# Kernel tuning notes

Hardware: AMD Instinct MI355X
Metric: run time of the kernel (lower is better)

Reference implementation:

```python
import jax, jax.numpy as jnp
import numpy as np

B, S, H, DH, HQ, HKV = 2, 1024, 2048, 128, 16, 4
E, K, I, IS = 16, 4, 1024, 1024
EPS = 1e-5
ROPE_BASE = 10000.0
ROUTED_SCALE = 1.0


def rmsnorm(x, w):
    v = jnp.mean(x.astype(jnp.float32) ** 2, axis=-1, keepdims=True)
    return (x.astype(jnp.float32) * jax.lax.rsqrt(v + EPS)).astype(x.dtype) * w


def rope(x, cos, sin):
    x1, x2 = jnp.split(x, 2, axis=-1)
    return jnp.concatenate([x1 * cos - x2 * sin, x2 * cos + x1 * sin], axis=-1)


def setup_inputs() -> dict:
    key = jax.random.key(0)
    ks = jax.random.split(key, 24)
    s = 0.02
    inp = {}
    inp['x'] = jax.random.normal(ks[0], (B, S, H), dtype=jnp.float32)
    inp['in_ln_w'] = jnp.ones((H,), jnp.float32)
    inp['wq'] = jax.random.normal(ks[1], (H, HQ * DH), jnp.float32) * s
    inp['bq'] = jax.random.normal(ks[2], (HQ * DH,), jnp.float32) * s
    inp['wk'] = jax.random.normal(ks[3], (H, HKV * DH), jnp.float32) * s
    inp['bk'] = jax.random.normal(ks[4], (HKV * DH,), jnp.float32) * s
    inp['wv'] = jax.random.normal(ks[5], (H, HKV * DH), jnp.float32) * s
    inp['bv'] = jax.random.normal(ks[6], (HKV * DH,), jnp.float32) * s
    inp['qn_w'] = jnp.ones((DH,), jnp.float32)
    inp['kn_w'] = jnp.ones((DH,), jnp.float32)
    inp['wo'] = jax.random.normal(ks[7], (HQ * DH, H), jnp.float32) * s
    inp['post_ln_w'] = jnp.ones((H,), jnp.float32)
    inp['gate_w'] = jax.random.normal(ks[8], (E, H), jnp.float32) * s
    inp['gate_b'] = jax.random.normal(ks[9], (E,), jnp.float32) * s
    inp['wg'] = jax.random.normal(ks[10], (E, H, I), jnp.float32) * s
    inp['wu'] = jax.random.normal(ks[11], (E, H, I), jnp.float32) * s
    inp['wd'] = jax.random.normal(ks[12], (E, I, H), jnp.float32) * s
    inp['swg'] = jax.random.normal(ks[13], (H, IS), jnp.float32) * s
    inp['swu'] = jax.random.normal(ks[14], (H, IS), jnp.float32) * s
    inp['swd'] = jax.random.normal(ks[15], (IS, H), jnp.float32) * s
    return inp


def reference(x, in_ln_w, wq, bq, wk, bk, wv, bv, qn_w, kn_w, wo, post_ln_w,
              gate_w, gate_b, wg, wu, wd, swg, swu, swd):
    # ---- attention block ----
    res = x
    h = rmsnorm(x, in_ln_w)
    q = (h @ wq + bq).reshape(B, S, HQ, DH)
    k = (h @ wk + bk).reshape(B, S, HKV, DH)
    v = (h @ wv + bv).reshape(B, S, HKV, DH)
    q = rmsnorm(q, qn_w)  # per-head QK norm over head_dim
    k = rmsnorm(k, kn_w)
    inv_freq = 1.0 / (ROPE_BASE ** (jnp.arange(0, DH, 2, dtype=jnp.float32) / DH))  # [DH/2]
    fr = jnp.arange(S, dtype=jnp.float32)[:, None] * inv_freq[None, :]  # [S, DH/2]
    cos = jnp.cos(fr)[None, :, None, :]
    sin = jnp.sin(fr)[None, :, None, :]
    q = rope(q, cos, sin)
    k = rope(k, cos, sin)
    g = HQ // HKV
    k = jnp.repeat(k, g, axis=2)  # GQA expand to [B,S,HQ,DH]
    v = jnp.repeat(v, g, axis=2)
    scores = jnp.einsum('bqhd,bkhd->bhqk', q, k) * (DH ** -0.5)
    causal = jnp.tril(jnp.ones((S, S), dtype=bool))
    scores = jnp.where(causal[None, None], scores, jnp.float32(-1e30))
    attn = jax.nn.softmax(scores, axis=-1)
    o = jnp.einsum('bhqk,bkhd->bqhd', attn, v).reshape(B, S, HQ * DH) @ wo
    x = res + o
    # ---- MoE block ----
    res = x
    h = rmsnorm(x, post_ln_w)
    ht = h.reshape(B * S, H)  # [T, H]
    logits = ht.astype(jnp.float32) @ gate_w.T  # fp32 router
    scr = jax.nn.sigmoid(logits)  # [T, E]
    choice = scr + gate_b[None, :]  # noaux_tc: bias only for selection
    _, topi = jax.lax.top_k(choice, K)  # [T, K]
    tw = jnp.take_along_axis(scr, topi, axis=-1)  # unbiased combine weights
    tw = tw / (jnp.sum(tw, axis=-1, keepdims=True) + 1e-20)  # norm_topk_prob
    tw = tw * ROUTED_SCALE
    cw = jnp.sum(jax.nn.one_hot(topi, E, dtype=jnp.float32) * tw[..., None], axis=1)  # [T, E]
    a = jnp.einsum('th,ehi->eti', ht, wg)
    b = jnp.einsum('th,ehi->eti', ht, wu)
    inter = jax.nn.silu(a) * b * cw.T[:, :, None]  # scale before down-proj
    routed = jnp.einsum('eti,eih->th', inter, wd)
    shared = (jax.nn.silu(ht @ swg) * (ht @ swu)) @ swd
    out = res + (routed + shared).reshape(B, S, H)
    return out
```

## Files before the change

### kernel.cpp

```cpp
#include <hip/hip_runtime.h>
#include <math.h>

typedef unsigned short u16;
typedef __attribute__((ext_vector_type(8))) short short8;
typedef __attribute__((ext_vector_type(4))) float f32x4;

#define B_ 2
#define S_ 1024
#define H_ 2048
#define DH_ 128
#define HQ_ 16
#define HKV_ 4
#define E_ 16
#define TOPK_ 4
#define I_ 1024
#define T_ (B_*S_)
#define NQKV_ 3072
#define NSEG_ 17
#define NA_ (T_*TOPK_ + T_)
#define K3_ 6144
#define MAXTILE 97

#define QPLANE ((long)B_*HQ_*S_*DH_)
#define KPLANE ((long)B_*HKV_*S_*DH_)
#define VPLANE ((long)B_*HKV_*DH_*S_)

__device__ __forceinline__ float bf2f(u16 u){
  union { unsigned int i; float f; } x; x.i = ((unsigned int)u) << 16; return x.f;
}
__device__ __forceinline__ u16 f2bf(float f){
  union { float f; unsigned int i; } x; x.f = f;
  unsigned int r = x.i + 0x7fffu + ((x.i >> 16) & 1u);
  return (u16)(r >> 16);
}
__device__ __forceinline__ void split_bf(float v, u16& hi, u16& lo){
  hi = f2bf(v);
  lo = f2bf(v - bf2f(hi));
}

__device__ __forceinline__ void gld_lds16(const void* g, void* l){
  __builtin_amdgcn_global_load_lds(
      (const __attribute__((address_space(1))) unsigned int*)g,
      (__attribute__((address_space(3))) unsigned int*)l, 16, 0, 0);
}

__device__ __forceinline__ f32x4 mfma_bf16(short8 a, short8 b, f32x4 c){
  return __builtin_amdgcn_mfma_f32_16x16x32_bf16(a, b, c, 0, 0, 0);
}

__global__ void k_transpose(const float* __restrict__ in, u16* __restrict__ out,
                            int R, int C, int rowMul, int rowOff,
                            long inBatch, long outBatch, int split3)
{
  __shared__ float tile[64][65];
  const float* inp = in + (long)blockIdx.z * inBatch;
  u16* outp = out + (long)blockIdx.z * outBatch;
  int c0 = blockIdx.x * 64, r0 = blockIdx.y * 64;
  int tid = threadIdx.x;
  int qc = (tid & 15) * 4;
  int rr = tid >> 4;
#pragma unroll
  for (int p = 0; p < 4; p++){
    int r = p*16 + rr;
    float4 v = *(const float4*)(inp + (long)(r0 + r)*C + c0 + qc);
    tile[r][qc] = v.x; tile[r][qc+1] = v.y; tile[r][qc+2] = v.z; tile[r][qc+3] = v.w;
  }
  __syncthreads();
  int rl = (tid & 15) * 4;
  int cw = tid >> 4;
#pragma unroll
  for (int p = 0; p < 4; p++){
    int c = p*16 + cw;
    float v0 = tile[rl][c], v1 = tile[rl+1][c], v2 = tile[rl+2][c], v3 = tile[rl+3][c];
    if (split3){
      ushort4 hi, lo;
      split_bf(v0, hi.x, lo.x); split_bf(v1, hi.y, lo.y);
      split_bf(v2, hi.z, lo.z); split_bf(v3, hi.w, lo.w);
      long base = (long)((c0 + c)*rowMul + rowOff) * (3*R) + r0 + rl;
      *(ushort4*)(outp + base)       = hi;
      *(ushort4*)(outp + base + R)   = lo;
      *(ushort4*)(outp + base + 2*R) = hi;
    } else {
      ushort4 hi = { f2bf(v0), f2bf(v1), f2bf(v2), f2bf(v3) };
      *(ushort4*)(outp + (long)((c0 + c)*rowMul + rowOff) * R + r0 + rl) = hi;
    }
  }
}

__global__ void k_rmsnorm(const float* __restrict__ x, const float* __restrict__ w,
                          u16* __restrict__ out3)
{
  int t = blockIdx.x;
  const float4* r4 = (const float4*)(x + (long)t * H_);
  const float4* w4 = (const float4*)w;
  float4 a = r4[threadIdx.x], b = r4[threadIdx.x + 256];
  float ss = a.x*a.x + a.y*a.y + a.z*a.z + a.w*a.w
           + b.x*b.x + b.y*b.y + b.z*b.z + b.w*b.w;
#pragma unroll
  for (int d = 1; d < 64; d <<= 1) ss += __shfl_xor(ss, d);
  __shared__ float red[4];
  int lane = threadIdx.x & 63, wv = threadIdx.x >> 6;
  if (lane == 0) red[wv] = ss;
  __syncthreads();
  ss = red[0] + red[1] + red[2] + red[3];
  float rs = rsqrtf(ss * (1.f / 2048.f) + 1e-5f);
  float4 wa = w4[threadIdx.x], wb = w4[threadIdx.x + 256];
  float va[8] = { a.x*rs*wa.x, a.y*rs*wa.y, a.z*rs*wa.z, a.w*rs*wa.w,
                  b.x*rs*wb.x, b.y*rs*wb.y, b.z*rs*wb.z, b.w*rs*wb.w };
  int pos0 = threadIdx.x*4, pos1 = 1024 + threadIdx.x*4;
  ushort4 hi0, lo0, hi1, lo1;
  split_bf(va[0], hi0.x, lo0.x); split_bf(va[1], hi0.y, lo0.y);
  split_bf(va[2], hi0.z, lo0.z); split_bf(va[3], hi0.w, lo0.w);
  split_bf(va[4], hi1.x, lo1.x); split_bf(va[5], hi1.y, lo1.y);
  split_bf(va[6], hi1.z, lo1.z); split_bf(va[7], hi1.w, lo1.w);
  u16* row = out3 + (long)t * K3_;
  *(ushort4*)(row + pos0) = hi0;        *(ushort4*)(row + pos1) = hi1;
  *(ushort4*)(row + 2048 + pos0) = hi0; *(ushort4*)(row + 2048 + pos1) = hi1;
  *(ushort4*)(row + 4096 + pos0) = lo0; *(ushort4*)(row + 4096 + pos1) = lo1;
}

__global__ void k_add_rmsnorm(const float* __restrict__ x, const float* __restrict__ p0,
                              const float* __restrict__ w, float* __restrict__ xa,
                              u16* __restrict__ out1, float* __restrict__ outf)
{
  int t = blockIdx.x;
  long base = (long)t * H_;
  const float4* x4 = (const float4*)(x + base);
  const float4* a4 = (const float4*)(p0 + base);
  const float4* w4 = (const float4*)w;
  int i0 = threadIdx.x, i1 = threadIdx.x + 256;
  float4 xv0 = x4[i0], xv1 = x4[i1];
  float4 av0 = a4[i0], av1 = a4[i1];
  float4 s0, s1;
  s0.x = xv0.x+av0.x; s0.y = xv0.y+av0.y; s0.z = xv0.z+av0.z; s0.w = xv0.w+av0.w;
  s1.x = xv1.x+av1.x; s1.y = xv1.y+av1.y; s1.z = xv1.z+av1.z; s1.w = xv1.w+av1.w;
  *(float4*)(xa + base + i0*4) = s0;
  *(float4*)(xa + base + i1*4) = s1;
  float ss = s0.x*s0.x + s0.y*s0.y + s0.z*s0.z + s0.w*s0.w
           + s1.x*s1.x + s1.y*s1.y + s1.z*s1.z + s1.w*s1.w;
#pragma unroll
  for (int d = 1; d < 64; d <<= 1) ss += __shfl_xor(ss, d);
  __shared__ float red[4];
  int lane = threadIdx.x & 63, wv = threadIdx.x >> 6;
  if (lane == 0) red[wv] = ss;
  __syncthreads();
  ss = red[0] + red[1] + red[2] + red[3];
  float rs = rsqrtf(ss * (1.f / 2048.f) + 1e-5f);
  float4 wa = w4[i0], wb = w4[i1];
  float va[8] = { s0.x*rs*wa.x, s0.y*rs*wa.y, s0.z*rs*wa.z, s0.w*rs*wa.w,
                  s1.x*rs*wb.x, s1.y*rs*wb.y, s1.z*rs*wb.z, s1.w*rs*wb.w };
  ushort4 q0 = { f2bf(va[0]), f2bf(va[1]), f2bf(va[2]), f2bf(va[3]) };
  ushort4 q1 = { f2bf(va[4]), f2bf(va[5]), f2bf(va[6]), f2bf(va[7]) };
  *(ushort4*)(out1 + base + i0*4) = q0;
  *(ushort4*)(out1 + base + i1*4) = q1;
  float4 oa = { va[0], va[1], va[2], va[3] };
  float4 ob = { va[4], va[5], va[6], va[7] };
  *(float4*)(outf + base + i0*4) = oa;
  *(float4*)(outf + base + i1*4) = ob;
}

__global__ void k_ropetab(float* __restrict__ tab){
  int s = blockIdx.x, i = threadIdx.x;
  double inv = pow(10000.0, -(double)i / 64.0);
  double fr = (double)s * inv;
  tab[s*128 + i]      = (float)cos(fr);
  tab[s*128 + 64 + i] = (float)sin(fr);
}

__global__ void k_ropenorm(const float* __restrict__ qkv, const float* __restrict__ biascat,
                           const float* __restrict__ qnw, const float* __restrict__ knw,
                           const float* __restrict__ tab,
                           u16* __restrict__ Q, u16* __restrict__ Kn, u16* __restrict__ Vt)
{
  long gw = (long)blockIdx.x * 4 + (threadIdx.x >> 6);
  int lane = threadIdx.x & 63;
  int hr = (int)(gw % 24);
  long bs = gw / 24;
  int s = (int)(bs % S_);
  int b = (int)(bs / S_);
  long ro = bs * NQKV_ + hr * DH_;
  float x1 = qkv[ro + lane] + biascat[hr*DH_ + lane];
  float x2 = qkv[ro + lane + 64] + biascat[hr*DH_ + lane + 64];
  if (hr < 20){
    float ss = x1*x1 + x2*x2;
#pragma unroll
    for (int d = 1; d < 64; d <<= 1) ss += __shfl_xor(ss, d);
    float rs = rsqrtf(ss * (1.f/128.f) + 1e-5f);
    const float* wn = (hr < 16) ? qnw : knw;
    float y1 = x1 * rs * wn[lane], y2 = x2 * rs * wn[lane + 64];
    float c = tab[s*128 + lane], sn = tab[s*128 + 64 + lane];
    float o1 = y1*c - y2*sn, o2 = y2*c + y1*sn;
    if (hr < 16){
      const float sc = 0.088388347648318447f;
      u16 h1,l1,h2,l2;
      split_bf(o1*sc, h1, l1); split_bf(o2*sc, h2, l2);
      u16* dst = Q + (((long)b*HQ_ + hr)*S_ + s) * DH_;
      dst[lane] = h1; dst[lane+64] = h2;
      dst[QPLANE + lane] = l1; dst[QPLANE + lane+64] = l2;
    } else {
      u16 h1,l1,h2,l2;
      split_bf(o1, h1, l1); split_bf(o2, h2, l2);
      u16* dst = Kn + (((long)b*HKV_ + (hr-16))*S_ + s) * DH_;
      dst[lane] = h1; dst[lane+64] = h2;
      dst[KPLANE + lane] = l1; dst[KPLANE + lane+64] = l2;
    }
  } else {
    u16 h1,l1,h2,l2;
    split_bf(x1, h1, l1); split_bf(x2, h2, l2);
    u16* dst = Vt + (((long)b*HKV_ + (hr-20))*DH_) * S_ + s;
    dst[(long)lane * S_]        = h1;
    dst[(long)(lane + 64) * S_] = h2;
    dst[VPLANE + (long)lane * S_]        = l1;
    dst[VPLANE + (long)(lane + 64) * S_] = l2;
  }
}

__launch_bounds__(256)
__global__ void k_attn(const u16* __restrict__ Q, const u16* __restrict__ Kn,
                       const u16* __restrict__ Vt, u16* __restrict__ O3)
{
  __shared__ u16 Ksh[32][128];
  __shared__ u16 Ksl[32][128];
  __shared__ u16 Vsh[128][32];
  __shared__ u16 Vsl[128][32];
  __shared__ u16 Psh[4][16][40];
  __shared__ u16 Psl[4][16][40];
  int qb = blockIdx.x, h = blockIdx.y, b = blockIdx.z;
  int kvh = h >> 2;
  int q0 = qb * 64;
  int tid = threadIdx.x, lane = tid & 63, w = tid >> 6;

  const u16* Qg = Q  + (((long)b*HQ_  + h  )*S_ + q0) * DH_;
  const u16* Kg = Kn + (((long)b*HKV_ + kvh)*S_) * DH_;
  const u16* Vg = Vt + (((long)b*HKV_ + kvh)*DH_) * S_;

  short8 qh[4], ql[4];
  {
    long qrow = w*16 + (lane & 15);
    int coff = (lane >> 4) << 3;
#pragma unroll
    for (int kst = 0; kst < 4; kst++){
      qh[kst] = *(const short8*)(Qg + qrow*DH_ + kst*32 + coff);
      ql[kst] = *(const short8*)(Qg + QPLANE + qrow*DH_ + kst*32 + coff);
    }
  }

  f32x4 o[8];
#pragma unroll
  for (int nt = 0; nt < 8; nt++) o[nt] = (f32x4){0.f,0.f,0.f,0.f};
  float mrow[4] = {-INFINITY,-INFINITY,-INFINITY,-INFINITY};
  float lrow[4] = {0.f,0.f,0.f,0.f};

  for (int j = 0; j <= 2*qb + 1; ++j){
#pragma unroll
    for (int it = 0; it < 2; ++it){
      int flat = it*256 + tid;
      int r = flat >> 4, pc = flat & 15;
      int c = pc ^ (((r&7) << 1) | ((r >> 3) & 1));
      long gsrc = ((long)(j*32 + r))*DH_ + c*8;
      gld_lds16(Kg + gsrc,          &Ksh[0][0] + (it*256 + (w<<6))*8);
      gld_lds16(Kg + KPLANE + gsrc, &Ksl[0][0] + (it*256 + (w<<6))*8);
    }
#pragma unroll
    for (int it = 0; it < 2; ++it){
      int flat = it*256 + tid;
      int r = flat >> 2, pc = flat & 3;
      int c = pc ^ (r & 3);
      long gsrc = (long)r*S_ + j*32 + c*8;
      gld_lds16(Vg + gsrc,          &Vsh[0][0] + (it*256 + (w<<6))*8);
      gld_lds16(Vg + VPLANE + gsrc, &Vsl[0][0] + (it*256 + (w<<6))*8);
    }
    __syncthreads();

    f32x4 s[2];
#pragma unroll
    for (int nt = 0; nt < 2; nt++) s[nt] = (f32x4){0.f,0.f,0.f,0.f};
#pragma unroll
    for (int kst = 0; kst < 4; kst++){
#pragma unroll
      for (int nt = 0; nt < 2; nt++){
        int br = nt*16 + (lane & 15);
        int bc = (kst*4 + (lane >> 4)) ^ (((br&7)<<1) | ((br>>3)&1));
        short8 kh = *(const short8*)&Ksh[br][bc*8];
        short8 kl = *(const short8*)&Ksl[br][bc*8];
        s[nt] = mfma_bf16(qh[kst], kh, s[nt]);
        s[nt] = mfma_bf16(qh[kst], kl, s[nt]);
        s[nt] = mfma_bf16(ql[kst], kh, s[nt]);
      }
    }
    if (j >= 2*qb){
#pragma unroll
      for (int nt = 0; nt < 2; nt++){
        int key = j*32 + nt*16 + (lane & 15);
#pragma unroll
        for (int r = 0; r < 4; r++){
          int qrow = q0 + w*16 + ((lane >> 4) << 2) + r;
          if (key > qrow) s[nt][r] = -1e30f;
        }
      }
    }
    float pm[4];
#pragma unroll
    for (int r = 0; r < 4; r++) pm[r] = fmaxf(s[0][r], s[1][r]);
#pragma unroll
    for (int d = 1; d < 16; d <<= 1){
#pragma unroll
      for (int r = 0; r < 4; r++) pm[r] = fmaxf(pm[r], __shfl_xor(pm[r], d));
    }
    float alpha[4];
#pragma unroll
    for (int r = 0; r < 4; r++){
      float mn = fmaxf(mrow[r], pm[r]);
      alpha[r] = __expf(mrow[r] - mn);
      mrow[r] = mn;
    }
    float psum[4] = {0.f,0.f,0.f,0.f};
#pragma unroll
    for (int nt = 0; nt < 2; nt++){
#pragma unroll
      for (int r = 0; r < 4; r++){
        float p = __expf(s[nt][r] - mrow[r]);
        psum[r] += p;
        u16 ph, pl; split_bf(p, ph, pl);
        int qr = ((lane>>4)<<2) + r, kc = nt*16 + (lane & 15);
        Psh[w][qr][kc] = ph;
        Psl[w][qr][kc] = pl;
      }
    }
#pragma unroll
    for (int d = 1; d < 16; d <<= 1){
#pragma unroll
      for (int r = 0; r < 4; r++) psum[r] += __shfl_xor(psum[r], d);
    }
#pragma unroll
    for (int r = 0; r < 4; r++) lrow[r] = lrow[r]*alpha[r] + psum[r];
#pragma unroll
    for (int nt = 0; nt < 8; nt++)
#pragma unroll
      for (int r = 0; r < 4; r++) o[nt][r] *= alpha[r];

    {
      short8 pah = *(const short8*)&Psh[w][lane & 15][(lane >> 4) << 3];
      short8 pal = *(const short8*)&Psl[w][lane & 15][(lane >> 4) << 3];
#pragma unroll
      for (int nt = 0; nt < 8; nt++){
        int br = nt*16 + (lane & 15);
        int bc = (lane >> 4) ^ (br & 3);
        short8 vh = *(const short8*)&Vsh[br][bc*8];
        short8 vl = *(const short8*)&Vsl[br][bc*8];
        o[nt] = mfma_bf16(pah, vh, o[nt]);
        o[nt] = mfma_bf16(pah, vl, o[nt]);
        o[nt] = mfma_bf16(pal, vh, o[nt]);
      }
    }
    __syncthreads();
  }
  float inv_[4];
#pragma unroll
  for (int r = 0; r < 4; r++) inv_[r] = 1.f / lrow[r];
#pragma unroll
  for (int nt = 0; nt < 8; nt++){
#pragma unroll
    for (int r = 0; r < 4; r++){
      long row = (long)b*S_ + q0 + w*16 + ((lane >> 4) << 2) + r;
      float val = o[nt][r] * inv_[r];
      u16 hi, lo; split_bf(val, hi, lo);
      long base = row*K3_ + h*DH_ + nt*16 + (lane & 15);
      O3[base]        = hi;
      O3[base + 2048] = hi;
      O3[base + 4096] = lo;
    }
  }
}

template<int KITERS>
__launch_bounds__(256)
__global__ void k_gemm_d(const u16* __restrict__ A, const u16* __restrict__ Bm,
                         float* __restrict__ C, int N, int Kstride)
{
  __shared__ u16 LDS[4*8192];
  int tid = threadIdx.x;
  int lane = tid & 63, w = tid >> 6;
  int wr = w >> 1, wc = w & 1;
  int n0 = blockIdx.x * 128;
  int m0 = blockIdx.y * 128;

  const u16* aS[2]; const u16* bS[2];
#pragma unroll
  for (int it = 0; it < 2; ++it){
    int c = w + it*4;
    int row = c*16 + (lane >> 2);
    int ps = (lane & 3) ^ ((row >> 1) & 3);
    aS[it] = A + (long)(m0 + row) * Kstride + ps*8;
    bS[it] = Bm + (long)(n0 + row) * Kstride + ps*8;
  }

  int offA[4], offB[4];
#pragma unroll
  for (int m = 0; m < 4; m++){
    int r = wr*64 + m*16 + (lane & 15);
    int ps = (lane >> 4) ^ ((r >> 1) & 3);
    offA[m] = r*32 + ps*8;
  }
#pragma unroll
  for (int n = 0; n < 4; n++){
    int r = wc*64 + n*16 + (lane & 15);
    int ps = (lane >> 4) ^ ((r >> 1) & 3);
    offB[n] = 4096 + r*32 + ps*8;
  }

  f32x4 acc[4][4];
#pragma unroll
  for (int m = 0; m < 4; m++)
#pragma unroll
    for (int n = 0; n < 4; n++) acc[m][n] = (f32x4){0.f,0.f,0.f,0.f};

  auto STAGE = [&](int Tt){
    int kb = Tt * 32;
    int db = (Tt & 3) * 8192;
#pragma unroll
    for (int it = 0; it < 2; ++it){
      gld_lds16(aS[it] + kb, &LDS[db + (w + it*4)*512]);
      gld_lds16(bS[it] + kb, &LDS[db + 4096 + (w + it*4)*512]);
    }
  };

  STAGE(0); STAGE(1); STAGE(2);

  for (int T = 0; T < KITERS; ++T){
    if (T + 3 < KITERS) STAGE(T + 3);
    int rem = KITERS - 1 - T;
    if (rem >= 3)      asm volatile("s_waitcnt vmcnt(12)" ::: "memory");
    else if (rem == 2) asm volatile("s_waitcnt vmcnt(8)"  ::: "memory");
    else if (rem == 1) asm volatile("s_waitcnt vmcnt(4)"  ::: "memory");
    else               asm volatile("s_waitcnt vmcnt(0)"  ::: "memory");
    __builtin_amdgcn_s_barrier();
    __builtin_amdgcn_sched_barrier(0);
    const u16* L = &LDS[(T & 3) * 8192];
    short8 af[4], bfv[4];
#pragma unroll
    for (int m = 0; m < 4; m++) af[m]  = *(const short8*)(L + offA[m]);
#pragma unroll
    for (int n = 0; n < 4; n++) bfv[n] = *(const short8*)(L + offB[n]);
#pragma unroll
    for (int m = 0; m < 4; m++)
#pragma unroll
      for (int n = 0; n < 4; n++)
        acc[m][n] = mfma_bf16(af[m], bfv[n], acc[m][n]);
    asm volatile("s_waitcnt lgkmcnt(0)" ::: "memory");
    __builtin_amdgcn_sched_barrier(0);
    __builtin_amdgcn_s_barrier();
  }

#pragma unroll
  for (int m = 0; m < 4; m++){
    int row0 = m0 + wr*64 + m*16 + ((lane >> 4) << 2);
#pragma unroll
    for (int n = 0; n < 4; n++){
      int col = n0 + wc*64 + n*16 + (lane & 15);
#pragma unroll
      for (int r = 0; r < 4; r++)
        C[(long)(row0 + r)*N + col] = acc[m][n][r];
    }
  }
}

template<int MODE>
__launch_bounds__(256)
__global__ void k_gemm_g(const u16* __restrict__ A, const u16* __restrict__ Bm,
                         void* __restrict__ Cout,
                         int Kloop, long segStrideB,
                         const int* __restrict__ segStart, const int* __restrict__ segCount,
                         const int* __restrict__ tileSeg, const int* __restrict__ tileMb,
                         const int* __restrict__ meta,
                         const int* __restrict__ assignTS, const float* __restrict__ assignW,
                         u16* __restrict__ downb)
{
  __shared__ u16 As[128][64];
  __shared__ u16 Bs[128][64];
  int tid = threadIdx.x;
  int lane = tid & 63, w = tid >> 6;
  int wr = w >> 1, wc = w & 1;
  int n0 = blockIdx.x * 128;
  int ty = blockIdx.y;
  if (ty >= meta[0]) return;
  int seg = tileSeg[ty], m0 = tileMb[ty] * 128;
  int segBase = segStart[seg];
  int cnt = segCount[seg];
  const u16* Bp = Bm + (long)seg * segStrideB;

  const u16* aS[4]; const u16* bS[4];
#pragma unroll
  for (int it = 0; it < 4; ++it){
    int flat = it*256 + tid;
    int r = flat >> 3, pc = flat & 7;
    int c = pc ^ (r & 7);
    long arow;
    if constexpr (MODE == 2) arow = (long)(assignTS[segBase + m0 + r] >> 3);
    else arow = (long)(segBase + m0 + r);
    aS[it] = A + arow * Kloop + c*8;
    bS[it] = Bp + (long)(n0 + r) * Kloop + c*8;
  }

  f32x4 acc[4][4];
#pragma unroll
  for (int m = 0; m < 4; m++)
#pragma unroll
    for (int n = 0; n < 4; n++) acc[m][n] = (f32x4){0.f,0.f,0.f,0.f};

  u16* AsF = &As[0][0]; u16* BsF = &Bs[0][0];
  for (int k0 = 0; k0 < Kloop; k0 += 64){
#pragma unroll
    for (int it = 0; it < 4; ++it){
      gld_lds16(aS[it] + k0, AsF + (it*256 + (w<<6))*8);
      gld_lds16(bS[it] + k0, BsF + (it*256 + (w<<6))*8);
    }
    __syncthreads();
#pragma unroll
    for (int kh = 0; kh < 2; ++kh){
      short8 af[4], bfv[4];
#pragma unroll
      for (int m = 0; m < 4; m++){
        int r = wr*64 + m*16 + (lane & 15);
        int c = (kh*4 + (lane >> 4)) ^ (r & 7);
        af[m] = *(const short8*)&As[r][c*8];
      }
#pragma unroll
      for (int n = 0; n < 4; n++){
        int r = wc*64 + n*16 + (lane & 15);
        int c = (kh*4 + (lane >> 4)) ^ (r & 7);
        bfv[n] = *(const short8*)&Bs[r][c*8];
      }
#pragma unroll
      for (int m = 0; m < 4; m++)
#pragma unroll
        for (int n = 0; n < 4; n++)
          acc[m][n] = mfma_bf16(af[m], bfv[n], acc[m][n]);
    }
    __syncthreads();
  }

  if constexpr (MODE == 2){
    u16* inter = (u16*)Cout;
#pragma unroll
    for (int m = 0; m < 4; m++){
      int row0 = m0 + wr*64 + m*16 + ((lane >> 4) << 2);
#pragma unroll
      for (int n = 0; n < 4; n++){
        f32x4 a = acc[m][n];
        float ov[4];
#pragma unroll
        for (int r = 0; r < 4; r++) ov[r] = __shfl_xor(a[r], 1);
        if ((lane & 1) == 0){
          int colp = (n0 + wc*64 + n*16 + (lane & 15)) >> 1;
#pragma unroll
          for (int r = 0; r < 4; r++){
            int rl = row0 + r;
            if (rl < cnt){
              int pos = segBase + rl;
              float g = a[r], u = ov[r];
              float val = (g / (1.f + __expf(-g))) * u * assignW[pos];
              inter[(long)pos*I_ + colp] = f2bf(val);
            }
          }
        }
      }
    }
  } else {
#pragma unroll
    for (int m = 0; m < 4; m++){
      int row0 = m0 + wr*64 + m*16 + ((lane >> 4) << 2);
#pragma unroll
      for (int n = 0; n < 4; n++){
        int col = n0 + wc*64 + n*16 + (lane & 15);
#pragma unroll
        for (int r = 0; r < 4; r++){
          int rl = row0 + r;
          if (rl < cnt){
            int ts = assignTS[segBase + rl];
            downb[((long)(ts >> 3)*5 + (ts & 7))*H_ + col] = f2bf(acc[m][n][r]);
          }
        }
      }
    }
  }
}

__global__ void k_router(const float* __restrict__ ht, const float* __restrict__ gw,
                         const float* __restrict__ gb, int* __restrict__ tok_e,
                         float* __restrict__ tok_w, int* __restrict__ counts)
{
  int t = blockIdx.x * 4 + (threadIdx.x >> 6);
  int lane = threadIdx.x & 63;
  const float4* row4 = (const float4*)(ht + (long)t * H_);
  float acc[16];
#pragma unroll
  for (int e = 0; e < 16; e++) acc[e] = 0.f;
#pragma unroll
  for (int it = 0; it < 8; it++){
    float4 rv = row4[lane + 64*it];
#pragma unroll
    for (int e = 0; e < 16; e++){
      float4 gv = *(const float4*)(gw + (long)e*H_ + (lane + 64*it)*4);
      acc[e] += rv.x*gv.x + rv.y*gv.y + rv.z*gv.z + rv.w*gv.w;
    }
  }
#pragma unroll
  for (int d = 1; d < 64; d <<= 1){
#pragma unroll
    for (int e = 0; e < 16; e++) acc[e] += __shfl_xor(acc[e], d);
  }
  if (lane == 0){
    float scr[16], ch[16];
#pragma unroll
    for (int e = 0; e < 16; e++){
      float s = 1.f / (1.f + __expf(-acc[e]));
      scr[e] = s; ch[e] = s + gb[e];
    }
    int sel[4]; float tw[4]; float sum = 0.f;
#pragma unroll
    for (int k = 0; k < 4; k++){
      int best = -1; float bv = -1e30f;
      for (int e = 0; e < 16; e++){
        bool used = false;
        for (int j = 0; j < k; j++) if (sel[j] == e) used = true;
        if (!used && ch[e] > bv){ bv = ch[e]; best = e; }
      }
      sel[k] = best; tw[k] = scr[best]; sum += scr[best];
    }
    float inv = 1.f / (sum + 1e-20f);
#pragma unroll
    for (int k = 0; k < 4; k++){
      tok_e[t*4 + k] = sel[k];
      tok_w[t*4 + k] = tw[k] * inv;
      atomicAdd(&counts[sel[k]], 1);
    }
  }
}

__global__ void k_scan(const int* __restrict__ counts, int* __restrict__ segStart,
                       int* __restrict__ segCount, int* __restrict__ cursor,
                       int* __restrict__ tileSeg, int* __restrict__ tileMb,
                       int* __restrict__ meta)
{
  if (threadIdx.x == 0){
    int off = 0, nt = 0;
    for (int e = 0; e < 16; e++){
      segStart[e] = off; segCount[e] = counts[e]; cursor[e] = off;
      for (int mb = 0; mb*128 < counts[e]; ++mb){ tileSeg[nt] = e; tileMb[nt] = mb; nt++; }
      off += counts[e];
    }
    segStart[16] = T_*TOPK_; segCount[16] = T_;
    for (int mb = 0; mb < 16; ++mb){ tileSeg[nt] = 16; tileMb[nt] = mb; nt++; }
    meta[0] = nt;
  }
}

__global__ void k_scatter(const int* __restrict__ tok_e, const float* __restrict__ tok_w,
                          int* __restrict__ cursor, int* __restrict__ assignTS,
                          float* __restrict__ assignW)
{
  int t = blockIdx.x*256 + threadIdx.x;
  if (t < T_){
    for (int k = 0; k < 4; k++){
      int e = tok_e[t*4 + k];
      int pos = atomicAdd(&cursor[e], 1);
      assignTS[pos] = t*8 + k;
      assignW[pos] = tok_w[t*4 + k];
    }
    assignTS[T_*TOPK_ + t] = t*8 + 4;
    assignW[T_*TOPK_ + t] = 1.f;
  }
}

__global__ void k_final(const float* __restrict__ xa, const u16* __restrict__ downb,
                        float* __restrict__ out)
{
  long i = ((long)blockIdx.x*256 + threadIdx.x) * 4;
  int t = (int)(i >> 11);
  int h = (int)(i & 2047);
  float4 r = *(const float4*)(xa + i);
  float a0 = r.x, a1 = r.y, a2 = r.z, a3 = r.w;
#pragma unroll
  for (int k = 0; k < 5; k++){
    const u16* d = downb + ((long)t*5 + k)*H_ + h;
    ushort4 v = *(const ushort4*)d;
    a0 += bf2f(v.x); a1 += bf2f(v.y); a2 += bf2f(v.z); a3 += bf2f(v.w);
  }
  float4 o = { a0, a1, a2, a3 };
  *(float4*)(out + i) = o;
}

extern "C" void kernel_launch(void* const* d_in, const int* in_sizes, int n_in,
                              void* d_out, int out_size, void* d_ws, size_t ws_size,
                              hipStream_t stream)
{
  (void)in_sizes; (void)n_in; (void)out_size; (void)ws_size;
  const float* x      = (const float*)d_in[0];
  const float* inlnw  = (const float*)d_in[1];
  const float* wq     = (const float*)d_in[2];
  const float* bq     = (const float*)d_in[3];
  const float* wk     = (const float*)d_in[4];
  const float* bk     = (const float*)d_in[5];
  const float* wv     = (const float*)d_in[6];
  const float* bv     = (const float*)d_in[7];
  const float* qnw    = (const float*)d_in[8];
  const float* knw    = (const float*)d_in[9];
  const float* wo     = (const float*)d_in[10];
  const float* postln = (const float*)d_in[11];
  const float* gatew  = (const float*)d_in[12];
  const float* gateb  = (const float*)d_in[13];
  const float* wg     = (const float*)d_in[14];
  const float* wu     = (const float*)d_in[15];
  const float* wdp    = (const float*)d_in[16];
  const float* swg    = (const float*)d_in[17];
  const float* swu    = (const float*)d_in[18];
  const float* swd    = (const float*)d_in[19];
  float* out = (float*)d_out;

  char* ws = (char*)d_ws;
  size_t off = 0;
  auto alloc = [&](size_t bytes) -> char* {
    char* p = ws + off; off += (bytes + 255) & ~(size_t)255; return p;
  };
  u16*   wqkv2   = (u16*)  alloc((size_t)NQKV_*K3_*2);
  u16*   wo2     = (u16*)  alloc((size_t)H_*K3_*2);
  u16*   wgu_t   = (u16*)  alloc((size_t)NSEG_*2048*2048*2);
  u16*   wd_t    = (u16*)  alloc((size_t)NSEG_*2048*1024*2);
  float* tab     = (float*)alloc((size_t)S_*128*4);
  float* biascat = (float*)alloc((size_t)NQKV_*4);
  float* xa      = (float*)alloc((size_t)T_*H_*4);
  int*   tok_e   = (int*)  alloc((size_t)T_*4*4);
  float* tok_w   = (float*)alloc((size_t)T_*4*4);
  int*   counts  = (int*)  alloc(32*4);
  int*   segStart= (int*)  alloc(32*4);
  int*   segCount= (int*)  alloc(32*4);
  int*   cursor  = (int*)  alloc(32*4);
  int*   tileSeg = (int*)  alloc(128*4);
  int*   tileMb  = (int*)  alloc(128*4);
  int*   meta    = (int*)  alloc(32*4);
  int*   assignTS= (int*)  alloc((size_t)NA_*4);
  float* assignW = (float*)alloc((size_t)NA_*4);
  char*  scrA    = alloc((size_t)T_*K3_*2);
  char*  scrBC   = alloc((size_t)2*T_*NQKV_*4);
  char*  scrD    = alloc((size_t)(2*QPLANE + 2*KPLANE + 2*VPLANE)*2);

  u16*   h2      = (u16*)scrA;
  u16*   attno2  = (u16*)scrA;
  u16*   inter   = (u16*)scrA;
  float* qkvp0   = (float*)scrBC;
  float* wop     = (float*)scrBC;
  u16*   Qb2     = (u16*)scrD;
  u16*   Kn2     = (u16*)(scrD + (size_t)2*QPLANE*2);
  u16*   Vt2     = (u16*)(scrD + (size_t)2*QPLANE*2 + (size_t)2*KPLANE*2);
  float* ht_f    = (float*)scrD;
  u16*   ht_b    = (u16*)(scrD + (size_t)T_*H_*4);
  u16*   downb   = (u16*)scrD;

  k_transpose<<<dim3(32,32,1),  256, 0, stream>>>(wq,  wqkv2, 2048, 2048, 1, 0,    0, 0, 1);
  k_transpose<<<dim3(8,32,1),   256, 0, stream>>>(wk,  wqkv2, 2048, 512,  1, 2048, 0, 0, 1);
  k_transpose<<<dim3(8,32,1),   256, 0, stream>>>(wv,  wqkv2, 2048, 512,  1, 2560, 0, 0, 1);
  k_transpose<<<dim3(32,32,1),  256, 0, stream>>>(wo,  wo2,   2048, 2048, 1, 0,    0, 0, 1);
  k_transpose<<<dim3(16,32,16), 256, 0, stream>>>(wg,  wgu_t, 2048, 1024, 2, 0, (long)2048*1024, (long)2048*2048, 0);
  k_transpose<<<dim3(16,32,16), 256, 0, stream>>>(wu,  wgu_t, 2048, 1024, 2, 1, (long)2048*1024, (long)2048*2048, 0);
  k_transpose<<<dim3(16,32,1),  256, 0, stream>>>(swg, wgu_t + (long)16*2048*2048, 2048, 1024, 2, 0, 0, 0, 0);
  k_transpose<<<dim3(16,32,1),  256, 0, stream>>>(swu, wgu_t + (long)16*2048*2048, 2048, 1024, 2, 1, 0, 0, 0);
  k_transpose<<<dim3(32,16,16), 256, 0, stream>>>(wdp, wd_t,  1024, 2048, 1, 0, (long)1024*2048, (long)2048*1024, 0);
  k_transpose<<<dim3(32,16,1),  256, 0, stream>>>(swd, wd_t + (long)16*2048*1024, 1024, 2048, 1, 0, 0, 0, 0);

  hipMemcpyAsync(biascat,        bq, 2048*4, hipMemcpyDeviceToDevice, stream);
  hipMemcpyAsync(biascat + 2048, bk, 512*4,  hipMemcpyDeviceToDevice, stream);
  hipMemcpyAsync(biascat + 2560, bv, 512*4,  hipMemcpyDeviceToDevice, stream);

  k_ropetab<<<S_, 64, 0, stream>>>(tab);
  k_rmsnorm<<<T_, 256, 0, stream>>>(x, inlnw, h2);

  k_gemm_d<192><<<dim3(24,16), 256, 0, stream>>>(h2, wqkv2, qkvp0, NQKV_, K3_);

  k_ropenorm<<<(T_*24)/4, 256, 0, stream>>>(qkvp0, biascat, qnw, knw, tab, Qb2, Kn2, Vt2);

  k_attn<<<dim3(S_/64, HQ_, B_), 256, 0, stream>>>(Qb2, Kn2, Vt2, attno2);

  k_gemm_d<192><<<dim3(16,16), 256, 0, stream>>>(attno2, wo2, wop, H_, K3_);

  k_add_rmsnorm<<<T_, 256, 0, stream>>>(x, wop, postln, xa, ht_b, ht_f);

  hipMemsetAsync(counts, 0, 32*4, stream);
  k_router<<<T_/4, 256, 0, stream>>>(ht_f, gatew, gateb, tok_e, tok_w, counts);
  k_scan<<<1, 64, 0, stream>>>(counts, segStart, segCount, cursor, tileSeg, tileMb, meta);
  k_scatter<<<(T_+255)/256, 256, 0, stream>>>(tok_e, tok_w, cursor, assignTS, assignW);

  k_gemm_g<2><<<dim3(16,MAXTILE), 256, 0, stream>>>(ht_b, wgu_t, inter,
      H_, (long)2048*2048, segStart, segCount, tileSeg, tileMb, meta, assignTS, assignW, nullptr);

  k_gemm_g<3><<<dim3(16,MAXTILE), 256, 0, stream>>>(inter, wd_t, nullptr,
      I_, (long)2048*1024, segStart, segCount, tileSeg, tileMb, meta, assignTS, assignW, downb);

  k_final<<<(T_*H_/4)/256, 256, 0, stream>>>(xa, downb, out);
}
```

Measured before the change: 855.2 us.

## Store split-bf16 operands once and remap K offsets in the dense GEMM

```diff
diff --git a/kernel.cpp b/kernel.cpp
--- a/kernel.cpp
+++ b/kernel.cpp
@@ -19,6 +19,7 @@
 #define NSEG_ 17
 #define NA_ (T_*TOPK_ + T_)
 #define K3_ 6144
+#define K2_ 4096
 #define MAXTILE 97
 
 #define QPLANE ((long)B_*HQ_*S_*DH_)
@@ -76,10 +77,9 @@
       ushort4 hi, lo;
       split_bf(v0, hi.x, lo.x); split_bf(v1, hi.y, lo.y);
       split_bf(v2, hi.z, lo.z); split_bf(v3, hi.w, lo.w);
-      long base = (long)((c0 + c)*rowMul + rowOff) * (3*R) + r0 + rl;
-      *(ushort4*)(outp + base)       = hi;
-      *(ushort4*)(outp + base + R)   = lo;
-      *(ushort4*)(outp + base + 2*R) = hi;
+      long base = (long)((c0 + c)*rowMul + rowOff) * (2*R) + r0 + rl;
+      *(ushort4*)(outp + base)     = hi;
+      *(ushort4*)(outp + base + R) = lo;
     } else {
       ushort4 hi = { f2bf(v0), f2bf(v1), f2bf(v2), f2bf(v3) };
       *(ushort4*)(outp + (long)((c0 + c)*rowMul + rowOff) * R + r0 + rl) = hi;
@@ -88,7 +88,7 @@
 }
 
 __global__ void k_rmsnorm(const float* __restrict__ x, const float* __restrict__ w,
-                          u16* __restrict__ out3)
+                          u16* __restrict__ out2)
 {
   int t = blockIdx.x;
   const float4* r4 = (const float4*)(x + (long)t * H_);
@@ -113,10 +113,9 @@
   split_bf(va[2], hi0.z, lo0.z); split_bf(va[3], hi0.w, lo0.w);
   split_bf(va[4], hi1.x, lo1.x); split_bf(va[5], hi1.y, lo1.y);
   split_bf(va[6], hi1.z, lo1.z); split_bf(va[7], hi1.w, lo1.w);
-  u16* row = out3 + (long)t * K3_;
+  u16* row = out2 + (long)t * K2_;
   *(ushort4*)(row + pos0) = hi0;        *(ushort4*)(row + pos1) = hi1;
-  *(ushort4*)(row + 2048 + pos0) = hi0; *(ushort4*)(row + 2048 + pos1) = hi1;
-  *(ushort4*)(row + 4096 + pos0) = lo0; *(ushort4*)(row + 4096 + pos1) = lo1;
+  *(ushort4*)(row + 2048 + pos0) = lo0; *(ushort4*)(row + 2048 + pos1) = lo1;
 }
 
 __global__ void k_add_rmsnorm(const float* __restrict__ x, const float* __restrict__ p0,
@@ -217,7 +216,7 @@
 
 __launch_bounds__(256)
 __global__ void k_attn(const u16* __restrict__ Q, const u16* __restrict__ Kn,
-                       const u16* __restrict__ Vt, u16* __restrict__ O3)
+                       const u16* __restrict__ Vt, u16* __restrict__ O2)
 {
   __shared__ u16 Ksh[32][128];
   __shared__ u16 Ksl[32][128];
@@ -225,7 +224,8 @@
   __shared__ u16 Vsl[128][32];
   __shared__ u16 Psh[4][16][40];
   __shared__ u16 Psl[4][16][40];
-  int qb = blockIdx.x, h = blockIdx.y, b = blockIdx.z;
+  int qb = (gridDim.x - 1) - blockIdx.x;
+  int h = blockIdx.y, b = blockIdx.z;
   int kvh = h >> 2;
   int q0 = qb * 64;
   int tid = threadIdx.x, lane = tid & 63, w = tid >> 6;
@@ -365,10 +365,9 @@
       long row = (long)b*S_ + q0 + w*16 + ((lane >> 4) << 2) + r;
       float val = o[nt][r] * inv_[r];
       u16 hi, lo; split_bf(val, hi, lo);
-      long base = row*K3_ + h*DH_ + nt*16 + (lane & 15);
-      O3[base]        = hi;
-      O3[base + 2048] = hi;
-      O3[base + 4096] = lo;
+      long base = row*K2_ + h*DH_ + nt*16 + (lane & 15);
+      O2[base]        = hi;
+      O2[base + 2048] = lo;
     }
   }
 }
@@ -376,7 +375,7 @@
 template<int KITERS>
 __launch_bounds__(256)
 __global__ void k_gemm_d(const u16* __restrict__ A, const u16* __restrict__ Bm,
-                         float* __restrict__ C, int N, int Kstride)
+                         float* __restrict__ C, int N)
 {
   __shared__ u16 LDS[4*8192];
   int tid = threadIdx.x;
@@ -391,8 +390,8 @@
     int c = w + it*4;
     int row = c*16 + (lane >> 2);
     int ps = (lane & 3) ^ ((row >> 1) & 3);
-    aS[it] = A + (long)(m0 + row) * Kstride + ps*8;
-    bS[it] = Bm + (long)(n0 + row) * Kstride + ps*8;
+    aS[it] = A + (long)(m0 + row) * K2_ + ps*8;
+    bS[it] = Bm + (long)(n0 + row) * K2_ + ps*8;
   }
 
   int offA[4], offB[4];
@@ -417,11 +416,13 @@
 
   auto STAGE = [&](int Tt){
     int kb = Tt * 32;
+    int kA = (kb < 2048) ? kb : kb - 2048;
+    int kB = (kb < 4096) ? kb : kb - 4096;
     int db = (Tt & 3) * 8192;
 #pragma unroll
     for (int it = 0; it < 2; ++it){
-      gld_lds16(aS[it] + kb, &LDS[db + (w + it*4)*512]);
-      gld_lds16(bS[it] + kb, &LDS[db + 4096 + (w + it*4)*512]);
+      gld_lds16(aS[it] + kA, &LDS[db + (w + it*4)*512]);
+      gld_lds16(bS[it] + kB, &LDS[db + 4096 + (w + it*4)*512]);
     }
   };
 
@@ -723,8 +724,8 @@
   auto alloc = [&](size_t bytes) -> char* {
     char* p = ws + off; off += (bytes + 255) & ~(size_t)255; return p;
   };
-  u16*   wqkv2   = (u16*)  alloc((size_t)NQKV_*K3_*2);
-  u16*   wo2     = (u16*)  alloc((size_t)H_*K3_*2);
+  u16*   wqkv2   = (u16*)  alloc((size_t)NQKV_*K2_*2);
+  u16*   wo2     = (u16*)  alloc((size_t)H_*K2_*2);
   u16*   wgu_t   = (u16*)  alloc((size_t)NSEG_*2048*2048*2);
   u16*   wd_t    = (u16*)  alloc((size_t)NSEG_*2048*1024*2);
   float* tab     = (float*)alloc((size_t)S_*128*4);
@@ -741,7 +742,7 @@
   int*   meta    = (int*)  alloc(32*4);
   int*   assignTS= (int*)  alloc((size_t)NA_*4);
   float* assignW = (float*)alloc((size_t)NA_*4);
-  char*  scrA    = alloc((size_t)T_*K3_*2);
+  char*  scrA    = alloc((size_t)NA_*I_*2);
   char*  scrBC   = alloc((size_t)2*T_*NQKV_*4);
   char*  scrD    = alloc((size_t)(2*QPLANE + 2*KPLANE + 2*VPLANE)*2);
 
@@ -775,13 +776,13 @@
   k_ropetab<<<S_, 64, 0, stream>>>(tab);
   k_rmsnorm<<<T_, 256, 0, stream>>>(x, inlnw, h2);
 
-  k_gemm_d<192><<<dim3(24,16), 256, 0, stream>>>(h2, wqkv2, qkvp0, NQKV_, K3_);
+  k_gemm_d<192><<<dim3(24,16), 256, 0, stream>>>(h2, wqkv2, qkvp0, NQKV_);
 
   k_ropenorm<<<(T_*24)/4, 256, 0, stream>>>(qkvp0, biascat, qnw, knw, tab, Qb2, Kn2, Vt2);
 
   k_attn<<<dim3(S_/64, HQ_, B_), 256, 0, stream>>>(Qb2, Kn2, Vt2, attno2);
 
-  k_gemm_d<192><<<dim3(16,16), 256, 0, stream>>>(attno2, wo2, wop, H_, K3_);
+  k_gemm_d<192><<<dim3(16,16), 256, 0, stream>>>(attno2, wo2, wop, H_);
 
   k_add_rmsnorm<<<T_, 256, 0, stream>>>(x, wop, postln, xa, ht_b, ht_f);
 
```

Result: no change. 841.9 us (-1.6%).
